# Kernel tuning notes

Measured on AMD Instinct MI355X. Metric: run time of the kernel, lower is better.

## Reference

```python
import jax, jax.numpy as jnp
import numpy as np

N_NODES = 100000
DIM = 256
N_SAMPLES = 64
N_CLASSES = 10


def setup_inputs() -> dict:
    key = jax.random.key(0)
    k1, k2, k3 = jax.random.split(key, 3)
    data = jax.random.normal(k1, (N_SAMPLES, DIM), dtype=jnp.float32)
    V = jax.random.uniform(k2, (N_NODES, DIM), dtype=jnp.float32)  # node matrix (torch.rand init)
    labels = jax.random.randint(k3, (N_SAMPLES,), 0, N_CLASSES)
    return {"data": data, "V": V, "labels": labels, "it": 0}


def reference(data, V, labels, it):
    # SOINN+ per-sample BMU search + BMU/sBMU weight pull, fixed node capacity.
    # eps schedules exactly as in ASOINN.forward.
    eps_b = 1.0 / (it + 2)
    eps_n = 1.0 / ((it + 1) * 100)

    def step(Vc, sample):
        # pairwise L2 distance of sample vs all nodes: [N]
        diff = sample[None, :] - Vc
        dists = jnp.sqrt(jnp.sum(diff * diff, axis=-1) + 1e-12)
        neg_vals, idx = jax.lax.top_k(-dists, 2)  # two smallest
        b, s = idx[0], idx[1]
        # update_bmu: V[b] += eps_b * (sample - V[b]); neighbor pull on sBMU
        Vc = Vc.at[b].add(eps_b * (sample - Vc[b]))
        Vc = Vc.at[s].add(eps_n * (sample - Vc[s]))
        return Vc, -neg_vals  # (b_dist, s_dist)

    V_final, bmu_dists = jax.lax.scan(step, V, data)
    return bmu_dists  # [N_SAMPLES, 2]
```

## Files before the change

kernel.cpp:

```cpp
#include <hip/hip_runtime.h>
#include <math.h>


#define N_NODES 100000
#define DIM     256
#define NS      64
#define NCH     1563
#define KC      32
#define NBMW    3125
#define CAP     4096
#define KL      192
#define KLS     136

typedef unsigned long long u64;

__device__ __forceinline__ u64 pk(float d, int i) {
  return ((u64)__float_as_uint(d) << 32) | (unsigned)i;
}
__device__ __forceinline__ u64 umin64(u64 a, u64 b) { return a < b ? a : b; }
__device__ __forceinline__ u64 umax64(u64 a, u64 b) { return a > b ? a : b; }
__device__ __forceinline__ void mrg2(u64& A0, u64& A1, u64 B0, u64 B1) {
  u64 m = umax64(A0, B0);
  A0 = umin64(A0, B0);
  A1 = umin64(umin64(A1, B1), m);
}

template <int C>
__device__ __forceinline__ u64 dpp64(u64 x) {
  unsigned lo = (unsigned)__builtin_amdgcn_update_dpp(
      (int)0xFFFFFFFF, (int)(unsigned)(x & 0xFFFFFFFFull), C, 0xF, 0xF, false);
  unsigned hi = (unsigned)__builtin_amdgcn_update_dpp(
      (int)0xFFFFFFFF, (int)(unsigned)(x >> 32), C, 0xF, 0xF, false);
  return ((u64)hi << 32) | lo;
}
template <int C>
__device__ __forceinline__ void dpp_round(u64& A0, u64& A1) {
  u64 B0 = dpp64<C>(A0);
  u64 B1 = dpp64<C>(A1);
  mrg2(A0, A1, B0, B1);
}

__global__ void k_xx(const float* __restrict__ X, float* __restrict__ XX) {
  int i = blockIdx.x, j = threadIdx.x;
  const float* xi = X + i * DIM;
  const float* xj = X + j * DIM;
  float acc = 0.f;
  for (int k = 0; k < DIM; k += 4) {
    float4 a = *(const float4*)(xi + k);
    float4 b = *(const float4*)(xj + k);
    acc += a.x * b.x + a.y * b.y + a.z * b.z + a.w * b.w;
  }
  XX[i * NS + j] = acc;
}

__global__ __launch_bounds__(256) void k_dist(const float* __restrict__ X,
                                              const float* __restrict__ V,
                                              const float* __restrict__ XX,
                                              float* __restrict__ P,
                                              float* __restrict__ PT,
                                              float* __restrict__ Q,
                                              u64* __restrict__ SUMC) {
  __shared__ float Xl[KC][68];
  __shared__ float Vl[KC][132];
  __shared__ float sq[128];
  const int tid = threadIdx.x;
  const int n0  = blockIdx.x * 128;
  const int ty  = tid >> 5;
  const int tx  = tid & 31;
  float acc[8][4];
#pragma unroll
  for (int i = 0; i < 8; i++)
#pragma unroll
    for (int u = 0; u < 4; u++) acc[i][u] = 0.f;
  float qa = 0.f;
  const int xsl = tid & 63;
  const int xkk = (tid >> 6) * 8;
  const int vn  = tid & 127;
  const int vkk = (tid >> 7) * 16;
  const bool vok = (n0 + vn < N_NODES);
  const float* vrow = V + (size_t)(n0 + vn) * DIM + vkk;
  const float* xrow = X + xsl * DIM + xkk;

  float4 xr0, xr1, vr[4];
  xr0 = *(const float4*)(xrow + 0);
  xr1 = *(const float4*)(xrow + 4);
#pragma unroll
  for (int m = 0; m < 4; m++)
    vr[m] = vok ? *(const float4*)(vrow + 4 * m) : make_float4(0.f, 0.f, 0.f, 0.f);

  for (int c = 0; c < 8; c++) {
    __syncthreads();
    Xl[xkk + 0][xsl] = xr0.x; Xl[xkk + 1][xsl] = xr0.y;
    Xl[xkk + 2][xsl] = xr0.z; Xl[xkk + 3][xsl] = xr0.w;
    Xl[xkk + 4][xsl] = xr1.x; Xl[xkk + 5][xsl] = xr1.y;
    Xl[xkk + 6][xsl] = xr1.z; Xl[xkk + 7][xsl] = xr1.w;
#pragma unroll
    for (int m = 0; m < 4; m++) {
      Vl[vkk + 4 * m + 0][vn] = vr[m].x; Vl[vkk + 4 * m + 1][vn] = vr[m].y;
      Vl[vkk + 4 * m + 2][vn] = vr[m].z; Vl[vkk + 4 * m + 3][vn] = vr[m].w;
    }
    __syncthreads();
    if (c + 1 < 8) {
      int kc = (c + 1) * KC;
      xr0 = *(const float4*)(xrow + kc);
      xr1 = *(const float4*)(xrow + kc + 4);
#pragma unroll
      for (int m = 0; m < 4; m++)
        vr[m] = vok ? *(const float4*)(vrow + kc + 4 * m)
                    : make_float4(0.f, 0.f, 0.f, 0.f);
    }
    if (tid < 128) {
      float qq = 0.f;
#pragma unroll 8
      for (int k = 0; k < KC; k++) { float t = Vl[k][tid]; qq += t * t; }
      qa += qq;
    }
#pragma unroll 4
    for (int k = 0; k < KC; k++) {
      float xs[8], vs[4];
      *(float4*)&xs[0] = *(const float4*)&Xl[k][ty * 8];
      *(float4*)&xs[4] = *(const float4*)&Xl[k][ty * 8 + 4];
      *(float4*)&vs[0] = *(const float4*)&Vl[k][tx * 4];
#pragma unroll
      for (int i = 0; i < 8; i++)
#pragma unroll
        for (int u = 0; u < 4; u++) acc[i][u] += xs[i] * vs[u];
    }
  }
  if (tid < 128) sq[tid] = qa;
  __syncthreads();
  if (tid < 128 && n0 + tid < N_NODES) Q[n0 + tid] = qa;
  float qs[4];
  *(float4*)&qs[0] = *(const float4*)&sq[tx * 4];
  const bool full = (n0 + 128) <= N_NODES;
#pragma unroll
  for (int i = 0; i < 8; i++) {
    int s = ty * 8 + i;
    float xn = XX[s * NS + s];
#pragma unroll
    for (int u = 0; u < 4; u++) acc[i][u] = xn - 2.f * acc[i][u] + qs[u];
    float* prow = P + (size_t)s * N_NODES + n0 + tx * 4;
    if (full) {
      *(float4*)(prow) = make_float4(acc[i][0], acc[i][1], acc[i][2], acc[i][3]);
    } else {
#pragma unroll
      for (int u = 0; u < 4; u++) {
        int n = n0 + tx * 4 + u;
        if (n < N_NODES) prow[u] = acc[i][u];
      }
    }
  }
#pragma unroll
  for (int u = 0; u < 4; u++) {
    int n = n0 + tx * 4 + u;
    if (n < N_NODES) {
      float* pt = PT + (size_t)n * NS + ty * 8;
      *(float4*)(pt)     = make_float4(acc[0][u], acc[1][u], acc[2][u], acc[3][u]);
      *(float4*)(pt + 4) = make_float4(acc[4][u], acc[5][u], acc[6][u], acc[7][u]);
    }
  }
#pragma unroll
  for (int i = 0; i < 8; i++) {
    int s = ty * 8 + i;
    u64 key = ~0ull;
#pragma unroll
    for (int u = 0; u < 4; u++) {
      int n = n0 + tx * 4 + u;
      if (n < N_NODES) key = umin64(key, pk(acc[i][u], n));
    }
#pragma unroll
    for (int off = 1; off <= 8; off <<= 1)
      key = umin64(key, (u64)__shfl_xor((unsigned long long)key, off, 64));
    if ((tx & 15) == 0) {
      int chunk = (n0 >> 6) + (tx >> 4);
      if (chunk < NCH) SUMC[(size_t)s * NCH + chunk] = key;
    }
  }
}

__global__ __launch_bounds__(1024) void k_build(const u64* __restrict__ SUMC,
                                                const float* __restrict__ P,
                                                u64* __restrict__ L) {
  __shared__ u64 A[CAP];
  __shared__ u64 Twave[16];
  __shared__ float Tsh;
  __shared__ int cnt;
  const int j = blockIdx.x, tid = threadIdx.x;
  const int w = tid >> 6, l = tid & 63;
  {
    int base = w * 98;
    u64 v0 = (base + l < NCH) ? SUMC[(size_t)j * NCH + base + l] : ~0ull;
    u64 v1 = (l < 34 && base + 64 + l < NCH)
                 ? SUMC[(size_t)j * NCH + base + 64 + l] : ~0ull;
    u64 s9 = ~0ull;
#pragma unroll
    for (int r = 0; r < 9; r++) {
      u64 m = umin64(v0, v1);
#pragma unroll
      for (int off = 1; off <= 32; off <<= 1)
        m = umin64(m, (u64)__shfl_xor((unsigned long long)m, off, 64));
      if (r == 8) { s9 = m; } else {
        if (v0 == m) v0 = ~0ull;
        if (v1 == m) v1 = ~0ull;
      }
    }
    if (l == 0) Twave[w] = s9;
  }
  __syncthreads();
  if (tid == 0) {
    u64 t = 0;
    for (int i = 0; i < 16; i++) t = umax64(t, Twave[i]);
    Tsh = __uint_as_float((unsigned)(t >> 32));
    cnt = 0;
  }
  __syncthreads();
  const float T = Tsh;
  const float* prow = P + (size_t)j * N_NODES;
  for (int n0 = tid * 4; n0 < N_NODES + 3; n0 += 4096) {
    float d[4];
    if (n0 + 3 < N_NODES) {
      float4 p = *(const float4*)(prow + n0);
      d[0] = p.x; d[1] = p.y; d[2] = p.z; d[3] = p.w;
    } else {
#pragma unroll
      for (int e = 0; e < 4; e++)
        d[e] = (n0 + e < N_NODES) ? prow[n0 + e] : INFINITY;
    }
#pragma unroll
    for (int e = 0; e < 4; e++) {
      if (d[e] <= T) {
        int pos = atomicAdd(&cnt, 1);
        if (pos < CAP) A[pos] = pk(d[e], n0 + e);
      }
    }
  }
  __syncthreads();
  int n = cnt; if (n > CAP) n = CAP;
  int M = 256; while (M < n) M <<= 1;
  for (int i = tid; i < M; i += 1024)
    if (i >= n) A[i] = ~0ull;
  __syncthreads();
  for (int k = 2; k <= M; k <<= 1)
    for (int s2 = k >> 1; s2 > 0; s2 >>= 1) {
      for (int i = tid; i < M; i += 1024) {
        int p = i ^ s2;
        if (p > i) {
          u64 a = A[i], b = A[p];
          bool up = ((i & k) == 0);
          if ((a > b) == up) { A[i] = b; A[p] = a; }
        }
      }
      __syncthreads();
    }
  for (int i = tid; i < KLS; i += 1024) L[(size_t)j * KL + i] = A[i];
}

__global__ __launch_bounds__(192) void k_seq(
    const float* __restrict__ PT, const float* __restrict__ Q,
    const float* __restrict__ XXg, const u64* __restrict__ L,
    const int* __restrict__ itp, float* __restrict__ out) {
  __shared__ float XXl[NS * 65];
  __shared__ float g[128][65];
  __shared__ float qv[128];
  __shared__ unsigned int bitmap[NBMW];
  __shared__ int tracked[128];
  __shared__ u64 cand16[NS][16];
  __shared__ float specg[4][6][NS];
  __shared__ float specq[4][6];
  __shared__ int   specid[4][6];
  __shared__ int ready[NS];
  __shared__ int done[NS];

  const int tid = threadIdx.x;
  const int wv = tid >> 6;
  const int lane = tid & 63;

  for (int i = tid; i < NS * NS; i += 192) {
    int r = i >> 6, c = i & 63;
    XXl[r * 65 + c] = XXg[i];
  }
  for (int i = tid; i < NBMW; i += 192) bitmap[i] = 0u;
  for (int i = tid; i < NS; i += 192) { ready[i] = 0; done[i] = 0; }
  __syncthreads();

  const int it = itp[0];
  const float eps_b = 1.0f / (float)(it + 2);
  const float eps_n = 1.0f / (float)((it + 1) * 100);
  const float xdl = XXl[lane * 65 + lane];

  if (wv == 0) {
    int ns = 0;
    int pw0 = -1, pw1 = -1, pw2 = -1, pw3 = -1;
    for (int j = 0; j < NS; j++) {
      while (__hip_atomic_load(&ready[j], __ATOMIC_ACQUIRE,
                               __HIP_MEMORY_SCOPE_WORKGROUP) == 0)
        __builtin_amdgcn_s_sleep(1);
      const int sb = j & 3;
      u64 ck = (lane < 16) ? cand16[j][lane] : ~0ull;
      float sgv[6], sqv[6]; int sid[6];
#pragma unroll
      for (int s = 0; s < 6; s++) {
        sgv[s] = specg[sb][s][lane];
        sid[s] = specid[sb][s];
        sqv[s] = specq[sb][s];
      }
      float gA = g[lane][j], gB = g[lane + 64][j];
      float qvA = qv[lane],  qvB = qv[lane + 64];
      int   tA = tracked[lane], tB = tracked[lane + 64];
      float xrow = XXl[j * 65 + lane];
      float xnj  = XXl[j * 65 + j];
      u64 A0 = ~0ull, A1 = ~0ull;
      {
        int id = (int)(unsigned)(ck & 0xFFFFFFFFull);
        bool ok = (ck != ~0ull) && id != pw0 && id != pw1 && id != pw2 && id != pw3;
        if (ok) { A0 = ck; }
      }
      if (lane < ns)      { float d = xnj - 2.f * gA + qvA; mrg2(A0, A1, pk(d, tA), ~0ull); }
      if (lane + 64 < ns) { float d = xnj - 2.f * gB + qvB; mrg2(A0, A1, pk(d, tB), ~0ull); }
      dpp_round<0x111>(A0, A1);
      dpp_round<0x112>(A0, A1);
      dpp_round<0x114>(A0, A1);
      dpp_round<0x118>(A0, A1);
      dpp_round<0x142>(A0, A1);
      dpp_round<0x143>(A0, A1);
      const int r0 = (int)(unsigned)__builtin_amdgcn_readlane(
          (int)(unsigned)(A0 & 0xFFFFFFFFull), 63);
      const int r1 = (int)(unsigned)__builtin_amdgcn_readlane(
          (int)(unsigned)(A1 & 0xFFFFFFFFull), 63);
      if (lane == 63) {
        float2 o;
        o.x = sqrtf(fmaxf(__uint_as_float((unsigned)(A0 >> 32)), 0.f) + 1e-12f);
        o.y = sqrtf(fmaxf(__uint_as_float((unsigned)(A1 >> 32)), 0.f) + 1e-12f);
        *(float2*)(out + j * 2) = o;
      }
      bool h0a = (lane < ns) && (tA == r0);
      bool h0b = (lane + 64 < ns) && (tB == r0);
      u64 mk0a = __ballot(h0a), mk0b = __ballot(h0b);
      bool new0 = (mk0a | mk0b) == 0ull;
      int sl0 = new0 ? ns
                     : (mk0a ? (__ffsll((unsigned long long)mk0a) - 1)
                             : (64 + __ffsll((unsigned long long)mk0b) - 1));
      bool h1a = (lane < ns) && (tA == r1);
      bool h1b = (lane + 64 < ns) && (tB == r1);
      u64 mk1a = __ballot(h1a), mk1b = __ballot(h1b);
      bool new1 = (mk1a | mk1b) == 0ull;
      int sl1 = new1 ? (ns + (new0 ? 1 : 0))
                     : (mk1a ? (__ffsll((unsigned long long)mk1a) - 1)
                             : (64 + __ffsll((unsigned long long)mk1b) - 1));
      bool hit0 = false, hit1 = false;
      float pv0 = 0.f, qq0 = 0.f, pv1 = 0.f, qq1 = 0.f;
#pragma unroll
      for (int s = 0; s < 6; s++) {
        bool h0 = (sid[s] == r0), h1 = (sid[s] == r1);
        pv0 = h0 ? sgv[s] : pv0;  qq0 = h0 ? sqv[s] : qq0;  hit0 |= h0;
        pv1 = h1 ? sgv[s] : pv1;  qq1 = h1 ? sqv[s] : qq1;  hit1 |= h1;
      }
      if (new0 && !hit0) { pv0 = PT[(size_t)r0 * NS + lane]; qq0 = Q[r0]; }
      if (new1 && !hit1) { pv1 = PT[(size_t)r1 * NS + lane]; qq1 = Q[r1]; }
      float gt0 = g[sl0][lane];
      float gt1 = g[sl1][lane];
      float gold0 = new0 ? (0.5f * (xdl + qq0 - pv0)) : gt0;
      float qold0 = new0 ? qq0
                         : __uint_as_float((unsigned)__builtin_amdgcn_readlane(
                               (int)__float_as_uint(sl0 < 64 ? qvA : qvB), sl0 & 63));
      float gj0 = __uint_as_float(
          (unsigned)__builtin_amdgcn_readlane((int)__float_as_uint(gold0), j));
      g[sl0][lane] = (1.f - eps_b) * gold0 + eps_b * xrow;
      if (lane == 0) {
        float om = 1.f - eps_b;
        qv[sl0] = om * om * qold0 + 2.f * eps_b * om * gj0 + eps_b * eps_b * xnj;
        tracked[sl0] = r0;
        if (new0) bitmap[r0 >> 5] |= 1u << (r0 & 31);
      }
      float gold1 = new1 ? (0.5f * (xdl + qq1 - pv1)) : gt1;
      float qold1 = new1 ? qq1
                         : __uint_as_float((unsigned)__builtin_amdgcn_readlane(
                               (int)__float_as_uint(sl1 < 64 ? qvA : qvB), sl1 & 63));
      float gj1 = __uint_as_float(
          (unsigned)__builtin_amdgcn_readlane((int)__float_as_uint(gold1), j));
      g[sl1][lane] = (1.f - eps_n) * gold1 + eps_n * xrow;
      if (lane == 0) {
        float on = 1.f - eps_n;
        qv[sl1] = on * on * qold1 + 2.f * eps_n * on * gj1 + eps_n * eps_n * xnj;
        tracked[sl1] = r1;
        if (new1) bitmap[r1 >> 5] |= 1u << (r1 & 31);
      }
      ns += (new0 ? 1 : 0) + (new1 ? 1 : 0);
      pw2 = pw0; pw3 = pw1; pw0 = r0; pw1 = r1;
      __hip_atomic_store(&done[j], 1, __ATOMIC_RELEASE,
                         __HIP_MEMORY_SCOPE_WORKGROUP);
    }
  } else {
    for (int t = (wv == 1 ? 0 : 1); t < NS; t += 2) {
      if (t >= 3) {
        while (__hip_atomic_load(&done[t - 3], __ATOMIC_ACQUIRE,
                                 __HIP_MEMORY_SCOPE_WORKGROUP) == 0)
          __builtin_amdgcn_s_sleep(1);
      }
      const u64* Lr = L + (size_t)t * KL;
      u64 e0 = Lr[lane], e1 = Lr[lane + 64];
      u64 e2 = (lane < 8) ? Lr[128 + lane] : ~0ull;
      int i0 = (int)(unsigned)(e0 & 0xFFFFFFFFull);
      int i1 = (int)(unsigned)(e1 & 0xFFFFFFFFull);
      int i2 = (int)(unsigned)(e2 & 0xFFFFFFFFull);
      bool t0 = (e0 == ~0ull) || ((bitmap[i0 >> 5] >> (i0 & 31)) & 1u);
      bool t1 = (e1 == ~0ull) || ((bitmap[i1 >> 5] >> (i1 & 31)) & 1u);
      bool t2 = (e2 == ~0ull) || ((bitmap[i2 >> 5] >> (i2 & 31)) & 1u);
      u64 um0 = ~__ballot(t0), um1 = ~__ballot(t1), um2 = ~__ballot(t2);
      u64 below = (1ull << lane) - 1;
      int c0n = __popcll((unsigned long long)um0);
      int c1n = __popcll((unsigned long long)um1);
      int rank0 = __popcll((unsigned long long)(um0 & below));
      int rank1 = c0n + __popcll((unsigned long long)(um1 & below));
      int rank2 = c0n + c1n + __popcll((unsigned long long)(um2 & below));
      if (!t0 && rank0 < 16) cand16[t][rank0] = e0;
      if (!t1 && rank1 < 16) cand16[t][rank1] = e1;
      if (!t2 && rank2 < 16) cand16[t][rank2] = e2;
      int U = c0n + c1n + __popcll((unsigned long long)um2);
      if (lane < 16 && lane >= U) cand16[t][lane] = ~0ull;
      const int sb = t & 3;
      int ids[6];
#pragma unroll
      for (int s = 0; s < 6; s++)
        ids[s] = (int)(unsigned)(cand16[t][s] & 0xFFFFFFFFull);
#pragma unroll
      for (int s = 0; s < 6; s++)
        specg[sb][s][lane] = PT[(size_t)ids[s] * NS + lane];
      if (lane < 6) {
        specid[sb][lane] = ids[lane];
        specq[sb][lane] = Q[ids[lane]];
      }
      __hip_atomic_store(&ready[t], 1, __ATOMIC_RELEASE,
                         __HIP_MEMORY_SCOPE_WORKGROUP);
    }
  }
}

extern "C" void kernel_launch(void* const* d_in, const int* in_sizes, int n_in,
                              void* d_out, int out_size, void* d_ws, size_t ws_size,
                              hipStream_t stream) {
  const float* X  = (const float*)d_in[0];
  const float* V  = (const float*)d_in[1];
  const int*  itp = (const int*)d_in[3];
  float* out = (float*)d_out;

  char* ws = (char*)d_ws;
  size_t off = 0;
  auto alloc = [&](size_t bytes) -> void* {
    size_t o = (off + 255) & ~(size_t)255;
    off = o + bytes;
    return (void*)(ws + o);
  };
  float* P    = (float*)alloc((size_t)NS * N_NODES * sizeof(float));
  float* PT   = (float*)alloc((size_t)NS * N_NODES * sizeof(float));
  float* Q    = (float*)alloc((size_t)N_NODES * sizeof(float));
  float* XXp  = (float*)alloc((size_t)NS * NS * sizeof(float));
  u64*   SUMC = (u64*)alloc((size_t)NS * NCH * sizeof(u64));
  u64*   Lst  = (u64*)alloc((size_t)NS * KL * sizeof(u64));

  k_xx   <<<NS, NS, 0, stream>>>(X, XXp);
  k_dist <<<(N_NODES + 127) / 128, 256, 0, stream>>>(X, V, XXp, P, PT, Q, SUMC);
  k_build<<<NS, 1024, 0, stream>>>(SUMC, P, Lst);
  k_seq  <<<1, 192, 0, stream>>>(PT, Q, XXp, Lst, itp, out);
}
```

Baseline: 308.3 us.

## Deepen producer lookahead in sequential BMU kernel with four prefetch waves

The sequential k_seq kernel grows from 2 to 4 producer wavefronts. Each producer now runs 5 samples ahead instead of 3, over 8 speculative buffers instead of 4. Recently updated node exclusion widens from 4 to 8 ids to stay correct at the deeper lookahead, and 10 candidate rows are prefetched per sample instead of 6. The consumer finds a speculative hit with a ballot over the prefetched ids and does an indexed LDS read, replacing per-slot register copies. The intent is to hide candidate-prep and PT-fetch latency from the serial consumer wave, at the cost of more LDS and a wider exclusion window that may push more candidates onto the slow global-fetch path.

```diff
diff --git a/kernel.cpp b/kernel.cpp
--- a/kernel.cpp
+++ b/kernel.cpp
@@ -11,6 +11,8 @@
 #define CAP     4096
 #define KL      192
 #define KLS     136
+#define NSP     10
+#define NPW     8
 
 typedef unsigned long long u64;
 
@@ -255,7 +257,7 @@
   for (int i = tid; i < KLS; i += 1024) L[(size_t)j * KL + i] = A[i];
 }
 
-__global__ __launch_bounds__(192) void k_seq(
+__global__ __launch_bounds__(320) void k_seq(
     const float* __restrict__ PT, const float* __restrict__ Q,
     const float* __restrict__ XXg, const u64* __restrict__ L,
     const int* __restrict__ itp, float* __restrict__ out) {
@@ -265,9 +267,9 @@
   __shared__ unsigned int bitmap[NBMW];
   __shared__ int tracked[128];
   __shared__ u64 cand16[NS][16];
-  __shared__ float specg[4][6][NS];
-  __shared__ float specq[4][6];
-  __shared__ int   specid[4][6];
+  __shared__ float specg[8][NSP][NS];
+  __shared__ float specq[8][NSP];
+  __shared__ int   specid[8][NSP];
   __shared__ int ready[NS];
   __shared__ int done[NS];
 
@@ -275,12 +277,12 @@
   const int wv = tid >> 6;
   const int lane = tid & 63;
 
-  for (int i = tid; i < NS * NS; i += 192) {
+  for (int i = tid; i < NS * NS; i += 320) {
     int r = i >> 6, c = i & 63;
     XXl[r * 65 + c] = XXg[i];
   }
-  for (int i = tid; i < NBMW; i += 192) bitmap[i] = 0u;
-  for (int i = tid; i < NS; i += 192) { ready[i] = 0; done[i] = 0; }
+  for (int i = tid; i < NBMW; i += 320) bitmap[i] = 0u;
+  for (int i = tid; i < NS; i += 320) { ready[i] = 0; done[i] = 0; }
   __syncthreads();
 
   const int it = itp[0];
@@ -290,20 +292,16 @@
 
   if (wv == 0) {
     int ns = 0;
-    int pw0 = -1, pw1 = -1, pw2 = -1, pw3 = -1;
+    int pw[NPW];
+#pragma unroll
+    for (int s = 0; s < NPW; s++) pw[s] = -1;
     for (int j = 0; j < NS; j++) {
       while (__hip_atomic_load(&ready[j], __ATOMIC_ACQUIRE,
                                __HIP_MEMORY_SCOPE_WORKGROUP) == 0)
         __builtin_amdgcn_s_sleep(1);
-      const int sb = j & 3;
+      const int sb = j & 7;
       u64 ck = (lane < 16) ? cand16[j][lane] : ~0ull;
-      float sgv[6], sqv[6]; int sid[6];
-#pragma unroll
-      for (int s = 0; s < 6; s++) {
-        sgv[s] = specg[sb][s][lane];
-        sid[s] = specid[sb][s];
-        sqv[s] = specq[sb][s];
-      }
+      int sidl = (lane < NSP) ? specid[sb][lane] : -2;
       float gA = g[lane][j], gB = g[lane + 64][j];
       float qvA = qv[lane],  qvB = qv[lane + 64];
       int   tA = tracked[lane], tB = tracked[lane + 64];
@@ -312,7 +310,9 @@
       u64 A0 = ~0ull, A1 = ~0ull;
       {
         int id = (int)(unsigned)(ck & 0xFFFFFFFFull);
-        bool ok = (ck != ~0ull) && id != pw0 && id != pw1 && id != pw2 && id != pw3;
+        bool ok = (ck != ~0ull);
+#pragma unroll
+        for (int s = 0; s < NPW; s++) ok = ok && (id != pw[s]);
         if (ok) { A0 = ck; }
       }
       if (lane < ns)      { float d = xnj - 2.f * gA + qvA; mrg2(A0, A1, pk(d, tA), ~0ull); }
@@ -347,14 +347,13 @@
       int sl1 = new1 ? (ns + (new0 ? 1 : 0))
                      : (mk1a ? (__ffsll((unsigned long long)mk1a) - 1)
                              : (64 + __ffsll((unsigned long long)mk1b) - 1));
-      bool hit0 = false, hit1 = false;
-      float pv0 = 0.f, qq0 = 0.f, pv1 = 0.f, qq1 = 0.f;
-#pragma unroll
-      for (int s = 0; s < 6; s++) {
-        bool h0 = (sid[s] == r0), h1 = (sid[s] == r1);
-        pv0 = h0 ? sgv[s] : pv0;  qq0 = h0 ? sqv[s] : qq0;  hit0 |= h0;
-        pv1 = h1 ? sgv[s] : pv1;  qq1 = h1 ? sqv[s] : qq1;  hit1 |= h1;
-      }
+      u64 mh0 = __ballot(sidl == r0);
+      u64 mh1 = __ballot(sidl == r1);
+      bool hit0 = mh0 != 0ull, hit1 = mh1 != 0ull;
+      int s0 = hit0 ? (__ffsll((unsigned long long)mh0) - 1) : 0;
+      int s1 = hit1 ? (__ffsll((unsigned long long)mh1) - 1) : 0;
+      float pv0 = specg[sb][s0][lane], qq0 = specq[sb][s0];
+      float pv1 = specg[sb][s1][lane], qq1 = specq[sb][s1];
       if (new0 && !hit0) { pv0 = PT[(size_t)r0 * NS + lane]; qq0 = Q[r0]; }
       if (new1 && !hit1) { pv1 = PT[(size_t)r1 * NS + lane]; qq1 = Q[r1]; }
       float gt0 = g[sl0][lane];
@@ -386,14 +385,16 @@
         if (new1) bitmap[r1 >> 5] |= 1u << (r1 & 31);
       }
       ns += (new0 ? 1 : 0) + (new1 ? 1 : 0);
-      pw2 = pw0; pw3 = pw1; pw0 = r0; pw1 = r1;
+#pragma unroll
+      for (int s = NPW - 1; s >= 2; s--) pw[s] = pw[s - 2];
+      pw[0] = r0; pw[1] = r1;
       __hip_atomic_store(&done[j], 1, __ATOMIC_RELEASE,
                          __HIP_MEMORY_SCOPE_WORKGROUP);
     }
   } else {
-    for (int t = (wv == 1 ? 0 : 1); t < NS; t += 2) {
-      if (t >= 3) {
-        while (__hip_atomic_load(&done[t - 3], __ATOMIC_ACQUIRE,
+    for (int t = wv - 1; t < NS; t += 4) {
+      if (t >= 5) {
+        while (__hip_atomic_load(&done[t - 5], __ATOMIC_ACQUIRE,
                                  __HIP_MEMORY_SCOPE_WORKGROUP) == 0)
           __builtin_amdgcn_s_sleep(1);
       }
@@ -418,15 +419,15 @@
       if (!t2 && rank2 < 16) cand16[t][rank2] = e2;
       int U = c0n + c1n + __popcll((unsigned long long)um2);
       if (lane < 16 && lane >= U) cand16[t][lane] = ~0ull;
-      const int sb = t & 3;
-      int ids[6];
-#pragma unroll
-      for (int s = 0; s < 6; s++)
+      const int sb = t & 7;
+      int ids[NSP];
+#pragma unroll
+      for (int s = 0; s < NSP; s++)
         ids[s] = (int)(unsigned)(cand16[t][s] & 0xFFFFFFFFull);
 #pragma unroll
-      for (int s = 0; s < 6; s++)
+      for (int s = 0; s < NSP; s++)
         specg[sb][s][lane] = PT[(size_t)ids[s] * NS + lane];
-      if (lane < 6) {
+      if (lane < NSP) {
         specid[sb][lane] = ids[lane];
         specq[sb][lane] = Q[ids[lane]];
       }
@@ -461,5 +462,5 @@
   k_xx   <<<NS, NS, 0, stream>>>(X, XXp);
   k_dist <<<(N_NODES + 127) / 128, 256, 0, stream>>>(X, V, XXp, P, PT, Q, SUMC);
   k_build<<<NS, 1024, 0, stream>>>(SUMC, P, Lst);
-  k_seq  <<<1, 192, 0, stream>>>(PT, Q, XXp, Lst, itp, out);
-}
+  k_seq  <<<1, 320, 0, stream>>>(PT, Q, XXp, Lst, itp, out);
+}
```

Result: no change. 308.8 us (+0.2%).
